# Kernel optimization log

Measured on AMD Instinct MI355X. Metric: run time of the kernel, lower is better.

## Reference

```python
import jax, jax.numpy as jnp
import numpy as np

N_USER = 200000
N_REPO = 100000
N_EDGE = 1500000
D = 128       # input feature dim for both node types
H = 128       # hidden_channels
O = 128       # out_channels


def _sage(x_src, x_dst, src_idx, dst_idx, n_dst, Wl, bl, Wr):
    # PyG SAGEConv: mean-aggregate source features per destination,
    # then lin_l(aggr) + lin_r(x_dst). lin_l has bias, lin_r does not.
    msg = x_src[src_idx]                                   # [E, d_src] gather
    s = jax.ops.segment_sum(msg, dst_idx, num_segments=n_dst)
    cnt = jax.ops.segment_sum(jnp.ones((src_idx.shape[0],), x_src.dtype),
                              dst_idx, num_segments=n_dst)
    mean = s / jnp.maximum(cnt, 1.0)[:, None]
    return mean @ Wl + bl + x_dst @ Wr


def setup_inputs() -> dict:
    key = jax.random.key(0)
    ks = jax.random.split(key, 16)
    s = 1.0 / np.sqrt(D)
    inp = {
        "x_user": jax.random.normal(ks[0], (N_USER, D), jnp.float32),
        "x_repo": jax.random.normal(ks[1], (N_REPO, D), jnp.float32),
        # row 0: user indices, row 1: repo indices
        "edge_stars": jnp.stack([
            jax.random.randint(ks[2], (N_EDGE,), 0, N_USER),
            jax.random.randint(ks[3], (N_EDGE,), 0, N_REPO),
        ]).astype(jnp.int64),
        # layer 1, edge type (user, stars, repo)
        "Wl1s": jax.random.uniform(ks[4], (D, H), jnp.float32, -s, s),
        "bl1s": jnp.zeros((H,), jnp.float32),
        "Wr1s": jax.random.uniform(ks[5], (D, H), jnp.float32, -s, s),
        # layer 1, edge type (repo, rev_stars, user)
        "Wl1r": jax.random.uniform(ks[6], (D, H), jnp.float32, -s, s),
        "bl1r": jnp.zeros((H,), jnp.float32),
        "Wr1r": jax.random.uniform(ks[7], (D, H), jnp.float32, -s, s),
        # layer 2, edge type (user, stars, repo)
        "Wl2s": jax.random.uniform(ks[8], (H, O), jnp.float32, -s, s),
        "bl2s": jnp.zeros((O,), jnp.float32),
        "Wr2s": jax.random.uniform(ks[9], (H, O), jnp.float32, -s, s),
        # layer 2, edge type (repo, rev_stars, user)
        "Wl2r": jax.random.uniform(ks[10], (H, O), jnp.float32, -s, s),
        "bl2r": jnp.zeros((O,), jnp.float32),
        "Wr2r": jax.random.uniform(ks[11], (H, O), jnp.float32, -s, s),
    }
    return inp


def reference(x_user, x_repo, edge_stars,
              Wl1s, bl1s, Wr1s, Wl1r, bl1r, Wr1r,
              Wl2s, bl2s, Wr2s, Wl2r, bl2r, Wr2r):
    u_idx, r_idx = edge_stars[0], edge_stars[1]
    # layer 1: stars (user->repo) updates repo; rev_stars (repo->user) updates user
    repo_h = jax.nn.relu(_sage(x_user, x_repo, u_idx, r_idx, N_REPO, Wl1s, bl1s, Wr1s))
    user_h = jax.nn.relu(_sage(x_repo, x_user, r_idx, u_idx, N_USER, Wl1r, bl1r, Wr1r))
    # layer 2
    repo_out = _sage(user_h, repo_h, u_idx, r_idx, N_REPO, Wl2s, bl2s, Wr2s)
    user_out = _sage(repo_h, user_h, r_idx, u_idx, N_USER, Wl2r, bl2r, Wr2r)
    return user_out, repo_out
```

## Files before the change

kernel.cpp:

```cpp
#include <hip/hip_runtime.h>
#include <stdint.h>

#define NUSER 200000
#define NREPO 100000
#define NEDGE 1500000

#define RB 98
#define UB 196
#define RCAP 17500
#define UCAP 9000

typedef unsigned short u16;
typedef unsigned int u32;
typedef __bf16 bf16x8 __attribute__((ext_vector_type(8)));
typedef float f32x4 __attribute__((ext_vector_type(4)));

#define OFF_RECR 0UL
#define OFF_RECU 6860000UL
#define OFF_B0   0UL
#define OFF_B1   51200256UL
#define OFF_B2   76800512UL
#define OFF_B3   128000768UL
#define OFF_COLR 153601024UL
#define OFF_COLU 159601024UL
#define OFF_POSR 165601024UL
#define OFF_POSU 166001024UL
#define OFF_WT   166801024UL
#define OFF_CUR  167063168UL
#define WS_NEEDED 167065568UL

#define ZR_B0 (OFF_B0 + 51200000UL)
#define ZR_B1 (OFF_B1 + 25600000UL)
#define ZR_B2 (OFF_B2 + 51200000UL)
#define ZR_B3 (OFF_B3 + 25600000UL)

__device__ __forceinline__ float bflo(u32 p) { return __uint_as_float(p << 16); }
__device__ __forceinline__ float bfhi(u32 p) { return __uint_as_float(p & 0xffff0000u); }
__device__ __forceinline__ u16 f2bf(float f) {
    u32 u = __float_as_uint(f);
    return (u16)((u + 0x7fffu + ((u >> 16) & 1u)) >> 16);
}
__device__ __forceinline__ bf16x8 as_bf16x8(uint4 u) {
    union { uint4 a; bf16x8 b; } x; x.a = u; return x.b;
}

__global__ void sentinel_kernel(float* out) { out[threadIdx.x] = 1234.5f; }

__global__ void init_kernel(char* __restrict__ ws) {
    int t = threadIdx.x;
    int* g = (int*)(ws + OFF_CUR);
    if (t < 300) g[t] = 0;
    if (t < 64) {
        ((u32*)(ws + ZR_B0))[t] = 0;
        ((u32*)(ws + ZR_B1))[t] = 0;
        ((u32*)(ws + ZR_B2))[t] = 0;
        ((u32*)(ws + ZR_B3))[t] = 0;
    }
}

__global__ void cvt_bf16_both(const float4* __restrict__ inA, uint2* __restrict__ outA, int n4A,
                              const float4* __restrict__ inB, uint2* __restrict__ outB, int n4B) {
    int i = blockIdx.x * blockDim.x + threadIdx.x;
    const float4* in; uint2* out; int idx;
    if (i < n4A) { in = inA; out = outA; idx = i; }
    else { in = inB; out = outB; idx = i - n4A; if (idx >= n4B) return; }
    float4 v = in[idx];
    uint2 o;
    o.x = (u32)f2bf(v.x) | ((u32)f2bf(v.y) << 16);
    o.y = (u32)f2bf(v.z) | ((u32)f2bf(v.w) << 16);
    out[idx] = o;
}

__global__ void wprep4_kernel(const float* __restrict__ Wl0, const float* __restrict__ Wr0,
                              const float* __restrict__ Wl1, const float* __restrict__ Wr1,
                              const float* __restrict__ Wl2, const float* __restrict__ Wr2,
                              const float* __restrict__ Wl3, const float* __restrict__ Wr3,
                              u16* __restrict__ Wt) {
    int which = blockIdx.x >> 7;
    const float* Wl = (which == 0) ? Wl0 : (which == 1) ? Wl1 : (which == 2) ? Wl2 : Wl3;
    const float* Wr = (which == 0) ? Wr0 : (which == 1) ? Wr1 : (which == 2) ? Wr2 : Wr3;
    int idx = (blockIdx.x & 127) * 256 + threadIdx.x;
    int n = idx >> 8, k = idx & 255;
    float v = (k < 128) ? Wl[k * 128 + n] : Wr[(k - 128) * 128 + n];
    Wt[which * 32768 + idx] = f2bf(v);
}

__device__ __forceinline__ bool detect_is64(const u32* e) {
    __shared__ int any_odd;
    int t = threadIdx.x;
    if (t == 0) any_odd = 0;
    __syncthreads();
    u32 acc = 0;
#pragma unroll
    for (int r = 0; r < 4; ++r) acc |= e[2 * (256 * r + t) + 1];
    if (acc != 0) any_odd = 1;
    __syncthreads();
    return !any_odd;
}

__global__ __launch_bounds__(256)
void passA_bin(const u32* __restrict__ e, u32* __restrict__ rec_r, u32* __restrict__ rec_u,
               int* __restrict__ gcur_r, int* __restrict__ gcur_u) {
    __shared__ int cntR[RB], cntU[UB], baseR[RB], baseU[UB];
    bool is64 = detect_is64(e);
    int t = threadIdx.x;
    for (int i = t; i < RB; i += 256) cntR[i] = 0;
    for (int i = t; i < UB; i += 256) cntU[i] = 0;
    __syncthreads();
    int base = blockIdx.x * 4096;
    int us[16], rs[16];
#pragma unroll
    for (int j = 0; j < 16; ++j) {
        int i = base + j * 256 + t;
        int u = -1, r = -1;
        if (i < NEDGE) {
            u = is64 ? (int)e[2 * i] : (int)e[i];
            r = is64 ? (int)e[2 * (NEDGE + i)] : (int)e[NEDGE + i];
        }
        us[j] = u; rs[j] = r;
        if (u >= 0) { atomicAdd(&cntR[r >> 10], 1); atomicAdd(&cntU[u >> 10], 1); }
    }
    __syncthreads();
    for (int i = t; i < RB; i += 256) baseR[i] = cntR[i] ? atomicAdd(&gcur_r[i], cntR[i]) : 0;
    for (int i = t; i < UB; i += 256) baseU[i] = cntU[i] ? atomicAdd(&gcur_u[i], cntU[i]) : 0;
    __syncthreads();
    for (int i = t; i < RB; i += 256) cntR[i] = 0;
    for (int i = t; i < UB; i += 256) cntU[i] = 0;
    __syncthreads();
#pragma unroll
    for (int j = 0; j < 16; ++j) {
        int u = us[j], r = rs[j];
        if (u >= 0) {
            int br = r >> 10, bu = u >> 10;
            int rk = baseR[br] + atomicAdd(&cntR[br], 1);
            if (rk < RCAP) rec_r[br * RCAP + rk] = ((u32)u << 10) | (u32)(r & 1023);
            int ku = baseU[bu] + atomicAdd(&cntU[bu], 1);
            if (ku < UCAP) rec_u[bu * UCAP + ku] = ((u32)r << 10) | (u32)(u & 1023);
        }
    }
}

__global__ void bucket_scan(const int* __restrict__ gcur_r, const int* __restrict__ gcur_u,
                            int* __restrict__ cb_r, int* __restrict__ cb_u) {
    __shared__ int s0[256], s1[256];
    int t = threadIdx.x;
    s0[t] = (t < RB) ? min(gcur_r[t], RCAP) : 0;
    __syncthreads();
    int* src = s0; int* dst = s1;
    for (int off = 1; off < 256; off <<= 1) {
        int x = src[t]; if (t >= off) x += src[t - off];
        dst[t] = x; __syncthreads();
        int* tmp = src; src = dst; dst = tmp;
    }
    if (t < RB) cb_r[t] = (t == 0) ? 0 : src[t - 1];
    __syncthreads();
    src[t] = 0; __syncthreads();
    s0[t] = (t < UB) ? min(gcur_u[t], UCAP) : 0;
    __syncthreads();
    src = s0; dst = s1;
    for (int off = 1; off < 256; off <<= 1) {
        int x = src[t]; if (t >= off) x += src[t - off];
        dst[t] = x; __syncthreads();
        int* tmp = src; src = dst; dst = tmp;
    }
    if (t < UB) cb_u[t] = (t == 0) ? 0 : src[t - 1];
}

__global__ __launch_bounds__(256)
void passB_build(const u32* __restrict__ rec_r, const u32* __restrict__ rec_u,
                 const int* __restrict__ gcur_r, const int* __restrict__ gcur_u,
                 const int* __restrict__ cb_r, const int* __restrict__ cb_u,
                 int* __restrict__ col_r, int* __restrict__ col_u,
                 int* __restrict__ pos_r, int* __restrict__ pos_u) {
    __shared__ int cnt[1024];
    __shared__ int excl[1024];
    __shared__ int sc0[256], sc1[256];
    int b = blockIdx.x;
    const u32* rec; int count, colbase, dstbase, ndst; int* col; int* pos;
    if (b < RB) {
        rec = rec_r + (size_t)b * RCAP; count = min(gcur_r[b], RCAP); colbase = cb_r[b];
        dstbase = b << 10; ndst = min(1024, NREPO - dstbase); col = col_r; pos = pos_r;
    } else {
        int c = b - RB;
        rec = rec_u + (size_t)c * UCAP; count = min(gcur_u[c], UCAP); colbase = cb_u[c];
        dstbase = c << 10; ndst = min(1024, NUSER - dstbase); col = col_u; pos = pos_u;
    }
    int t = threadIdx.x;
    for (int i = t; i < 1024; i += 256) cnt[i] = 0;
    __syncthreads();
    for (int i = t; i < count; i += 256) atomicAdd(&cnt[rec[i] & 1023], 1);
    __syncthreads();
    int c0 = cnt[t * 4], c1 = cnt[t * 4 + 1], c2 = cnt[t * 4 + 2], c3 = cnt[t * 4 + 3];
    int tsum = c0 + c1 + c2 + c3;
    sc0[t] = tsum; __syncthreads();
    int* src = sc0; int* dst = sc1;
    for (int off = 1; off < 256; off <<= 1) {
        int x = src[t]; if (t >= off) x += src[t - off];
        dst[t] = x; __syncthreads();
        int* tmp = src; src = dst; dst = tmp;
    }
    int exclT = src[t] - tsum;
    int e0 = exclT, e1 = e0 + c0, e2 = e1 + c1, e3 = e2 + c2;
    excl[t * 4] = e0; excl[t * 4 + 1] = e1; excl[t * 4 + 2] = e2; excl[t * 4 + 3] = e3;
    {
        int i = t * 4;
        if (i < ndst)     pos[dstbase + i]     = colbase + e1;
        if (i + 1 < ndst) pos[dstbase + i + 1] = colbase + e2;
        if (i + 2 < ndst) pos[dstbase + i + 2] = colbase + e3;
        if (i + 3 < ndst) pos[dstbase + i + 3] = colbase + e3 + c3;
    }
    __syncthreads();
    for (int i = t; i < 1024; i += 256) cnt[i] = 0;
    __syncthreads();
    for (int i = t; i < count; i += 256) {
        u32 rc = rec[i];
        int dl = rc & 1023;
        int rk = atomicAdd(&cnt[dl], 1);
        col[colbase + excl[dl] + rk] = (int)(rc >> 10);
    }
}

__global__ __launch_bounds__(256)
void gather_mean2(const u16* __restrict__ featA, const int* __restrict__ colA,
                  const int* __restrict__ posA, u16* __restrict__ outA, int ndstA, int nwaveA, int zrowA,
                  const u16* __restrict__ featB, const int* __restrict__ colB,
                  const int* __restrict__ posB, u16* __restrict__ outB, int ndstB, int zrowB) {
    int gw = (blockIdx.x * blockDim.x + threadIdx.x) >> 6;
    const u16* feat; const int* col; const int* pos; u16* outm; int ndst, dbase, zrow;
    if (gw < nwaveA) {
        feat = featA; col = colA; pos = posA; outm = outA; ndst = ndstA; dbase = gw * 2; zrow = zrowA;
    } else {
        feat = featB; col = colB; pos = posB; outm = outB; ndst = ndstB; dbase = (gw - nwaveA) * 2; zrow = zrowB;
    }
    int lane = threadIdx.x & 63;
    int h = lane >> 5, l5 = lane & 31, g2 = l5 >> 4, s = l5 & 15;
    int d = dbase + h;
    if (d >= ndst) return;

    int start = (d == 0) ? 0 : pos[d - 1];
    int end = pos[d];
    int deg = end - start;

    float acc[8];
#pragma unroll
    for (int k = 0; k < 8; ++k) acc[k] = 0.f;

#define LDROW(idx) (*(const uint4*)(feat + (size_t)(idx) * 128 + s * 8))
#define ACC4(a, b, c, dd) \
    acc[0] += (bflo(a.x) + bflo(b.x)) + (bflo(c.x) + bflo(dd.x)); \
    acc[1] += (bfhi(a.x) + bfhi(b.x)) + (bfhi(c.x) + bfhi(dd.x)); \
    acc[2] += (bflo(a.y) + bflo(b.y)) + (bflo(c.y) + bflo(dd.y)); \
    acc[3] += (bfhi(a.y) + bfhi(b.y)) + (bfhi(c.y) + bfhi(dd.y)); \
    acc[4] += (bflo(a.z) + bflo(b.z)) + (bflo(c.z) + bflo(dd.z)); \
    acc[5] += (bfhi(a.z) + bfhi(b.z)) + (bfhi(c.z) + bfhi(dd.z)); \
    acc[6] += (bflo(a.w) + bflo(b.w)) + (bflo(c.w) + bflo(dd.w)); \
    acc[7] += (bfhi(a.w) + bfhi(b.w)) + (bfhi(c.w) + bfhi(dd.w));

    if (deg > 0) {
        int mdeg = min(deg, 32);
        int cv = col[start + min(l5, mdeg - 1)];
        int hb = h * 32;
        for (int e0 = 0; e0 < mdeg; e0 += 8) {
            int i0 = e0 + g2, i1 = e0 + 2 + g2, i2 = e0 + 4 + g2, i3 = e0 + 6 + g2;
            int t0 = __shfl(cv, hb + i0, 64), t1 = __shfl(cv, hb + i1, 64);
            int t2 = __shfl(cv, hb + i2, 64), t3 = __shfl(cv, hb + i3, 64);
            int x0 = (i0 < deg) ? t0 : zrow, x1 = (i1 < deg) ? t1 : zrow;
            int x2 = (i2 < deg) ? t2 : zrow, x3 = (i3 < deg) ? t3 : zrow;
            uint4 v0 = LDROW(x0), v1 = LDROW(x1), v2 = LDROW(x2), v3 = LDROW(x3);
            ACC4(v0, v1, v2, v3)
        }
        for (int e = 32 + g2; e < deg; e += 2) {
            int idx = col[start + e];
            uint4 v = LDROW(idx);
            acc[0] += bflo(v.x); acc[1] += bfhi(v.x);
            acc[2] += bflo(v.y); acc[3] += bfhi(v.y);
            acc[4] += bflo(v.z); acc[5] += bfhi(v.z);
            acc[6] += bflo(v.w); acc[7] += bfhi(v.w);
        }
#pragma unroll
        for (int k = 0; k < 8; ++k) acc[k] += __shfl_xor(acc[k], 16, 64);
    }
#undef LDROW
#undef ACC4

    if (g2 == 0) {
        float inv = (deg > 0) ? 1.0f / (float)deg : 0.f;
        uint4 o;
        o.x = (u32)f2bf(acc[0] * inv) | ((u32)f2bf(acc[1] * inv) << 16);
        o.y = (u32)f2bf(acc[2] * inv) | ((u32)f2bf(acc[3] * inv) << 16);
        o.z = (u32)f2bf(acc[4] * inv) | ((u32)f2bf(acc[5] * inv) << 16);
        o.w = (u32)f2bf(acc[6] * inv) | ((u32)f2bf(acc[7] * inv) << 16);
        *(uint4*)(outm + (size_t)d * 128 + s * 8) = o;
    }
}

__global__ __launch_bounds__(256)
void transform_both(const u16* __restrict__ A_A, const u16* __restrict__ X_A,
                    const u16* __restrict__ Wt_A, const float* __restrict__ b_A,
                    u16* __restrict__ obf_A, float* __restrict__ of32_A, int N_A, int nblkA,
                    const u16* __restrict__ A_B, const u16* __restrict__ X_B,
                    const u16* __restrict__ Wt_B, const float* __restrict__ b_B,
                    u16* __restrict__ obf_B, float* __restrict__ of32_B, int N_B,
                    int do_relu) {
    __shared__ __align__(16) u16 sA[64][264];
    const u16* A; const u16* X; const u16* Wt; const float* bias;
    u16* out_bf; float* out_f32; int N, base;
    if ((int)blockIdx.x < nblkA) {
        A = A_A; X = X_A; Wt = Wt_A; bias = b_A; out_bf = obf_A; out_f32 = of32_A;
        N = N_A; base = blockIdx.x * 64;
    } else {
        A = A_B; X = X_B; Wt = Wt_B; bias = b_B; out_bf = obf_B; out_f32 = of32_B;
        N = N_B; base = (blockIdx.x - nblkA) * 64;
    }
    int tid = threadIdx.x;
    int w = tid >> 6, lane = tid & 63;
    int q = lane >> 4, n = lane & 15;
    int nb = w * 32;

    bf16x8 bfrag[2][8];
#pragma unroll
    for (int nt = 0; nt < 2; ++nt)
#pragma unroll
        for (int ks = 0; ks < 8; ++ks)
            bfrag[nt][ks] = as_bf16x8(*(const uint4*)(Wt + (size_t)(nb + nt * 16 + n) * 256 + ks * 32 + q * 8));
    float bv[2] = { bias[nb + n], bias[nb + 16 + n] };

    {
        int r = tid >> 2, c = tid & 3;
        int node = base + r;
        uint4 z = make_uint4(0, 0, 0, 0);
        uint4 va[4], vx[4];
        if (node < N) {
            const uint4* pa = (const uint4*)(A + (size_t)node * 128 + c * 32);
            const uint4* px = (const uint4*)(X + (size_t)node * 128 + c * 32);
#pragma unroll
            for (int j = 0; j < 4; ++j) { va[j] = pa[j]; vx[j] = px[j]; }
        } else {
#pragma unroll
            for (int j = 0; j < 4; ++j) { va[j] = z; vx[j] = z; }
        }
#pragma unroll
        for (int j = 0; j < 4; ++j) {
            *(uint4*)&sA[r][c * 32 + j * 8] = va[j];
            *(uint4*)&sA[r][128 + c * 32 + j * 8] = vx[j];
        }
    }
    __syncthreads();

    f32x4 zz = { 0.f, 0.f, 0.f, 0.f };
    f32x4 acc[4][2];
#pragma unroll
    for (int mt = 0; mt < 4; ++mt) { acc[mt][0] = zz; acc[mt][1] = zz; }

#pragma unroll
    for (int ks = 0; ks < 8; ++ks)
#pragma unroll
        for (int mt = 0; mt < 4; ++mt) {
            bf16x8 af = *(const bf16x8*)&sA[mt * 16 + n][ks * 32 + q * 8];
            acc[mt][0] = __builtin_amdgcn_mfma_f32_16x16x32_bf16(af, bfrag[0][ks], acc[mt][0], 0, 0, 0);
            acc[mt][1] = __builtin_amdgcn_mfma_f32_16x16x32_bf16(af, bfrag[1][ks], acc[mt][1], 0, 0, 0);
        }

#pragma unroll
    for (int mt = 0; mt < 4; ++mt) {
        int row0 = base + mt * 16 + q * 4;
#pragma unroll
        for (int nt = 0; nt < 2; ++nt) {
            int colg = nb + nt * 16 + n;
#pragma unroll
            for (int r = 0; r < 4; ++r) {
                int row = row0 + r;
                if (row < N) {
                    float v = acc[mt][nt][r] + bv[nt];
                    if (do_relu) v = fmaxf(v, 0.f);
                    if (out_bf) out_bf[(size_t)row * 128 + colg] = f2bf(v);
                    else        out_f32[(size_t)row * 128 + colg] = v;
                }
            }
        }
    }
}

extern "C" void kernel_launch(void* const* d_in, const int* in_sizes, int n_in,
                              void* d_out, int out_size, void* d_ws, size_t ws_size,
                              hipStream_t stream) {
    const float* x_user = (const float*)d_in[0];
    const float* x_repo = (const float*)d_in[1];
    const u32* edges = (const u32*)d_in[2];
    const float* Wl1s = (const float*)d_in[3], *bl1s = (const float*)d_in[4], *Wr1s = (const float*)d_in[5];
    const float* Wl1r = (const float*)d_in[6], *bl1r = (const float*)d_in[7], *Wr1r = (const float*)d_in[8];
    const float* Wl2s = (const float*)d_in[9], *bl2s = (const float*)d_in[10], *Wr2s = (const float*)d_in[11];
    const float* Wl2r = (const float*)d_in[12], *bl2r = (const float*)d_in[13], *Wr2r = (const float*)d_in[14];

    float* out_user = (float*)d_out;
    float* out_repo = (float*)d_out + (size_t)NUSER * 128;

    if (ws_size < WS_NEEDED) {
        hipLaunchKernelGGL(sentinel_kernel, dim3(1), dim3(256), 0, stream, out_user);
        return;
    }

    char* ws = (char*)d_ws;
    u32* rec_r = (u32*)(ws + OFF_RECR);
    u32* rec_u = (u32*)(ws + OFF_RECU);
    u16* B0 = (u16*)(ws + OFF_B0);
    u16* B1 = (u16*)(ws + OFF_B1);
    u16* B2 = (u16*)(ws + OFF_B2);
    u16* B3 = (u16*)(ws + OFF_B3);
    int* col_r = (int*)(ws + OFF_COLR);
    int* col_u = (int*)(ws + OFF_COLU);
    int* pos_r = (int*)(ws + OFF_POSR);
    int* pos_u = (int*)(ws + OFF_POSU);
    u16* wt1s = (u16*)(ws + OFF_WT);
    u16* wt1r = wt1s + 32768;
    u16* wt2s = wt1r + 32768;
    u16* wt2r = wt2s + 32768;
    int* gcur_r = (int*)(ws + OFF_CUR);
    int* gcur_u = (int*)(ws + OFF_CUR + 400);
    int* cb_r   = (int*)(ws + OFF_CUR + 1200);
    int* cb_u   = (int*)(ws + OFF_CUR + 1600);

    const int nblkR = (NREPO + 63) / 64;
    const int nblkU = (NUSER + 63) / 64;
    const int nwaveR = NREPO / 2;
    const int nwaveU = NUSER / 2;
    const int gblk = (nwaveR + nwaveU) / 4;

    hipLaunchKernelGGL(init_kernel, dim3(1), dim3(320), 0, stream, ws);
    hipLaunchKernelGGL(passA_bin, dim3(367), dim3(256), 0, stream, edges, rec_r, rec_u, gcur_r, gcur_u);
    hipLaunchKernelGGL(bucket_scan, dim3(1), dim3(256), 0, stream, gcur_r, gcur_u, cb_r, cb_u);
    hipLaunchKernelGGL(passB_build, dim3(RB + UB), dim3(256), 0, stream,
                       rec_r, rec_u, gcur_r, gcur_u, cb_r, cb_u, col_r, col_u, pos_r, pos_u);

    hipLaunchKernelGGL(wprep4_kernel, dim3(512), dim3(256), 0, stream,
                       Wl1s, Wr1s, Wl1r, Wr1r, Wl2s, Wr2s, Wl2r, Wr2r, wt1s);
    hipLaunchKernelGGL(cvt_bf16_both, dim3(37500), dim3(256), 0, stream,
                       (const float4*)x_user, (uint2*)B2, NUSER * 128 / 4,
                       (const float4*)x_repo, (uint2*)B3, NREPO * 128 / 4);

    hipLaunchKernelGGL(gather_mean2, dim3(gblk), dim3(256), 0, stream,
                       B2, col_r, pos_r, B1, NREPO, nwaveR, NUSER,
                       B3, col_u, pos_u, B0, NUSER, NREPO);
    hipLaunchKernelGGL(transform_both, dim3(nblkR + nblkU), dim3(256), 0, stream,
                       B1, B3, wt1s, bl1s, B1, (float*)nullptr, NREPO, nblkR,
                       B0, B2, wt1r, bl1r, B0, (float*)nullptr, NUSER,
                       1);

    hipLaunchKernelGGL(gather_mean2, dim3(gblk), dim3(256), 0, stream,
                       B0, col_r, pos_r, B3, NREPO, nwaveR, NUSER,
                       B1, col_u, pos_u, B2, NUSER, NREPO);
    hipLaunchKernelGGL(transform_both, dim3(nblkR + nblkU), dim3(256), 0, stream,
                       B3, B1, wt2s, bl2s, (u16*)nullptr, out_repo, NREPO, nblkR,
                       B2, B0, wt2r, bl2r, (u16*)nullptr, out_user, NUSER,
                       0);
}
```

Baseline: 680.2 us.

## Process multiple node tiles per transform block, shrink binning blocks, load gather indices directly

The transform kernel now handles four 64-row tiles per block and reloads the weight fragments only when the tile switches between the repo and user sides, which cuts the number of redundant weight-fragment loads. Edge binning uses 1024 edges per block instead of 4096, which launches more blocks to raise parallelism but adds more global atomics on the bucket cursors. The gather kernel reads neighbor indices straight from memory instead of broadcasting them with wave shuffles. This lowers shuffle work but issues more scattered index loads.

```diff
diff --git a/kernel.cpp b/kernel.cpp
--- a/kernel.cpp
+++ b/kernel.cpp
@@ -107,10 +107,10 @@
     for (int i = t; i < RB; i += 256) cntR[i] = 0;
     for (int i = t; i < UB; i += 256) cntU[i] = 0;
     __syncthreads();
-    int base = blockIdx.x * 4096;
-    int us[16], rs[16];
-#pragma unroll
-    for (int j = 0; j < 16; ++j) {
+    int base = blockIdx.x * 1024;
+    int us[4], rs[4];
+#pragma unroll
+    for (int j = 0; j < 4; ++j) {
         int i = base + j * 256 + t;
         int u = -1, r = -1;
         if (i < NEDGE) {
@@ -128,7 +128,7 @@
     for (int i = t; i < UB; i += 256) cntU[i] = 0;
     __syncthreads();
 #pragma unroll
-    for (int j = 0; j < 16; ++j) {
+    for (int j = 0; j < 4; ++j) {
         int u = us[j], r = rs[j];
         if (u >= 0) {
             int br = r >> 10, bu = u >> 10;
@@ -258,19 +258,17 @@
 
     if (deg > 0) {
         int mdeg = min(deg, 32);
-        int cv = col[start + min(l5, mdeg - 1)];
-        int hb = h * 32;
+        const int* cbase = col + start;
         for (int e0 = 0; e0 < mdeg; e0 += 8) {
             int i0 = e0 + g2, i1 = e0 + 2 + g2, i2 = e0 + 4 + g2, i3 = e0 + 6 + g2;
-            int t0 = __shfl(cv, hb + i0, 64), t1 = __shfl(cv, hb + i1, 64);
-            int t2 = __shfl(cv, hb + i2, 64), t3 = __shfl(cv, hb + i3, 64);
+            int t0 = cbase[i0], t1 = cbase[i1], t2 = cbase[i2], t3 = cbase[i3];
             int x0 = (i0 < deg) ? t0 : zrow, x1 = (i1 < deg) ? t1 : zrow;
             int x2 = (i2 < deg) ? t2 : zrow, x3 = (i3 < deg) ? t3 : zrow;
             uint4 v0 = LDROW(x0), v1 = LDROW(x1), v2 = LDROW(x2), v3 = LDROW(x3);
             ACC4(v0, v1, v2, v3)
         }
         for (int e = 32 + g2; e < deg; e += 2) {
-            int idx = col[start + e];
+            int idx = cbase[e];
             uint4 v = LDROW(idx);
             acc[0] += bflo(v.x); acc[1] += bfhi(v.x);
             acc[2] += bflo(v.y); acc[3] += bfhi(v.y);
@@ -294,87 +292,103 @@
     }
 }
 
+#define TILES_PER_BLK 4
 __global__ __launch_bounds__(256)
 void transform_both(const u16* __restrict__ A_A, const u16* __restrict__ X_A,
                     const u16* __restrict__ Wt_A, const float* __restrict__ b_A,
                     u16* __restrict__ obf_A, float* __restrict__ of32_A, int N_A, int nblkA,
                     const u16* __restrict__ A_B, const u16* __restrict__ X_B,
                     const u16* __restrict__ Wt_B, const float* __restrict__ b_B,
-                    u16* __restrict__ obf_B, float* __restrict__ of32_B, int N_B,
+                    u16* __restrict__ obf_B, float* __restrict__ of32_B, int N_B, int nblkB,
                     int do_relu) {
     __shared__ __align__(16) u16 sA[64][264];
-    const u16* A; const u16* X; const u16* Wt; const float* bias;
-    u16* out_bf; float* out_f32; int N, base;
-    if ((int)blockIdx.x < nblkA) {
-        A = A_A; X = X_A; Wt = Wt_A; bias = b_A; out_bf = obf_A; out_f32 = of32_A;
-        N = N_A; base = blockIdx.x * 64;
-    } else {
-        A = A_B; X = X_B; Wt = Wt_B; bias = b_B; out_bf = obf_B; out_f32 = of32_B;
-        N = N_B; base = (blockIdx.x - nblkA) * 64;
-    }
     int tid = threadIdx.x;
     int w = tid >> 6, lane = tid & 63;
     int q = lane >> 4, n = lane & 15;
     int nb = w * 32;
+    int r_st = tid >> 2, c_st = tid & 3;
 
     bf16x8 bfrag[2][8];
-#pragma unroll
-    for (int nt = 0; nt < 2; ++nt)
+    float bv[2];
+    int prev_side = -1;
+
+    int tile0 = blockIdx.x * TILES_PER_BLK;
+    int ntile = nblkA + nblkB;
+    for (int ti = 0; ti < TILES_PER_BLK; ++ti) {
+        int tile = tile0 + ti;
+        if (tile >= ntile) break;
+        int side = (tile < nblkA) ? 0 : 1;
+        const u16* A; const u16* X; const u16* Wt; const float* bias;
+        u16* out_bf; float* out_f32; int N, base;
+        if (side == 0) {
+            A = A_A; X = X_A; Wt = Wt_A; bias = b_A; out_bf = obf_A; out_f32 = of32_A;
+            N = N_A; base = tile * 64;
+        } else {
+            A = A_B; X = X_B; Wt = Wt_B; bias = b_B; out_bf = obf_B; out_f32 = of32_B;
+            N = N_B; base = (tile - nblkA) * 64;
+        }
+
+        if (side != prev_side) {
+            prev_side = side;
+#pragma unroll
+            for (int nt = 0; nt < 2; ++nt)
+#pragma unroll
+                for (int ks = 0; ks < 8; ++ks)
+                    bfrag[nt][ks] = as_bf16x8(*(const uint4*)(Wt + (size_t)(nb + nt * 16 + n) * 256 + ks * 32 + q * 8));
+            bv[0] = bias[nb + n]; bv[1] = bias[nb + 16 + n];
+        }
+
+        if (ti > 0) __syncthreads();
+        {
+            int node = base + r_st;
+            uint4 z = make_uint4(0, 0, 0, 0);
+            uint4 va[4], vx[4];
+            if (node < N) {
+                const uint4* pa = (const uint4*)(A + (size_t)node * 128 + c_st * 32);
+                const uint4* px = (const uint4*)(X + (size_t)node * 128 + c_st * 32);
+#pragma unroll
+                for (int j = 0; j < 4; ++j) { va[j] = pa[j]; vx[j] = px[j]; }
+            } else {
+#pragma unroll
+                for (int j = 0; j < 4; ++j) { va[j] = z; vx[j] = z; }
+            }
+#pragma unroll
+            for (int j = 0; j < 4; ++j) {
+                *(uint4*)&sA[r_st][c_st * 32 + j * 8] = va[j];
+                *(uint4*)&sA[r_st][128 + c_st * 32 + j * 8] = vx[j];
+            }
+        }
+        __syncthreads();
+
+        f32x4 zz = { 0.f, 0.f, 0.f, 0.f };
+        f32x4 acc[4][2];
+#pragma unroll
+        for (int mt = 0; mt < 4; ++mt) { acc[mt][0] = zz; acc[mt][1] = zz; }
+
 #pragma unroll
         for (int ks = 0; ks < 8; ++ks)
-            bfrag[nt][ks] = as_bf16x8(*(const uint4*)(Wt + (size_t)(nb + nt * 16 + n) * 256 + ks * 32 + q * 8));
-    float bv[2] = { bias[nb + n], bias[nb + 16 + n] };
-
-    {
-        int r = tid >> 2, c = tid & 3;
-        int node = base + r;
-        uint4 z = make_uint4(0, 0, 0, 0);
-        uint4 va[4], vx[4];
-        if (node < N) {
-            const uint4* pa = (const uint4*)(A + (size_t)node * 128 + c * 32);
-            const uint4* px = (const uint4*)(X + (size_t)node * 128 + c * 32);
-#pragma unroll
-            for (int j = 0; j < 4; ++j) { va[j] = pa[j]; vx[j] = px[j]; }
-        } else {
-#pragma unroll
-            for (int j = 0; j < 4; ++j) { va[j] = z; vx[j] = z; }
-        }
-#pragma unroll
-        for (int j = 0; j < 4; ++j) {
-            *(uint4*)&sA[r][c * 32 + j * 8] = va[j];
-            *(uint4*)&sA[r][128 + c * 32 + j * 8] = vx[j];
-        }
-    }
-    __syncthreads();
-
-    f32x4 zz = { 0.f, 0.f, 0.f, 0.f };
-    f32x4 acc[4][2];
-#pragma unroll
-    for (int mt = 0; mt < 4; ++mt) { acc[mt][0] = zz; acc[mt][1] = zz; }
-
-#pragma unroll
-    for (int ks = 0; ks < 8; ++ks)
+#pragma unroll
+            for (int mt = 0; mt < 4; ++mt) {
+                bf16x8 af = *(const bf16x8*)&sA[mt * 16 + n][ks * 32 + q * 8];
+                acc[mt][0] = __builtin_amdgcn_mfma_f32_16x16x32_bf16(af, bfrag[0][ks], acc[mt][0], 0, 0, 0);
+                acc[mt][1] = __builtin_amdgcn_mfma_f32_16x16x32_bf16(af, bfrag[1][ks], acc[mt][1], 0, 0, 0);
+            }
+
 #pragma unroll
         for (int mt = 0; mt < 4; ++mt) {
-            bf16x8 af = *(const bf16x8*)&sA[mt * 16 + n][ks * 32 + q * 8];
-            acc[mt][0] = __builtin_amdgcn_mfma_f32_16x16x32_bf16(af, bfrag[0][ks], acc[mt][0], 0, 0, 0);
-            acc[mt][1] = __builtin_amdgcn_mfma_f32_16x16x32_bf16(af, bfrag[1][ks], acc[mt][1], 0, 0, 0);
-        }
-
-#pragma unroll
-    for (int mt = 0; mt < 4; ++mt) {
-        int row0 = base + mt * 16 + q * 4;
-#pragma unroll
-        for (int nt = 0; nt < 2; ++nt) {
-            int colg = nb + nt * 16 + n;
-#pragma unroll
-            for (int r = 0; r < 4; ++r) {
-                int row = row0 + r;
-                if (row < N) {
-                    float v = acc[mt][nt][r] + bv[nt];
-                    if (do_relu) v = fmaxf(v, 0.f);
-                    if (out_bf) out_bf[(size_t)row * 128 + colg] = f2bf(v);
-                    else        out_f32[(size_t)row * 128 + colg] = v;
+            int row0 = base + mt * 16 + q * 4;
+#pragma unroll
+            for (int nt = 0; nt < 2; ++nt) {
+                int colg = nb + nt * 16 + n;
+#pragma unroll
+                for (int r = 0; r < 4; ++r) {
+                    int row = row0 + r;
+                    if (row < N) {
+                        float v = acc[mt][nt][r] + bv[nt];
+                        if (do_relu) v = fmaxf(v, 0.f);
+                        if (out_bf) out_bf[(size_t)row * 128 + colg] = f2bf(v);
+                        else        out_f32[(size_t)row * 128 + colg] = v;
+                    }
                 }
             }
         }
@@ -422,12 +436,15 @@
 
     const int nblkR = (NREPO + 63) / 64;
     const int nblkU = (NUSER + 63) / 64;
+    const int ntile = nblkR + nblkU;
+    const int tblk = (ntile + TILES_PER_BLK - 1) / TILES_PER_BLK;
     const int nwaveR = NREPO / 2;
     const int nwaveU = NUSER / 2;
     const int gblk = (nwaveR + nwaveU) / 4;
 
     hipLaunchKernelGGL(init_kernel, dim3(1), dim3(320), 0, stream, ws);
-    hipLaunchKernelGGL(passA_bin, dim3(367), dim3(256), 0, stream, edges, rec_r, rec_u, gcur_r, gcur_u);
+    hipLaunchKernelGGL(passA_bin, dim3((NEDGE + 1023) / 1024), dim3(256), 0, stream,
+                       edges, rec_r, rec_u, gcur_r, gcur_u);
     hipLaunchKernelGGL(bucket_scan, dim3(1), dim3(256), 0, stream, gcur_r, gcur_u, cb_r, cb_u);
     hipLaunchKernelGGL(passB_build, dim3(RB + UB), dim3(256), 0, stream,
                        rec_r, rec_u, gcur_r, gcur_u, cb_r, cb_u, col_r, col_u, pos_r, pos_u);
@@ -441,16 +458,16 @@
     hipLaunchKernelGGL(gather_mean2, dim3(gblk), dim3(256), 0, stream,
                        B2, col_r, pos_r, B1, NREPO, nwaveR, NUSER,
                        B3, col_u, pos_u, B0, NUSER, NREPO);
-    hipLaunchKernelGGL(transform_both, dim3(nblkR + nblkU), dim3(256), 0, stream,
+    hipLaunchKernelGGL(transform_both, dim3(tblk), dim3(256), 0, stream,
                        B1, B3, wt1s, bl1s, B1, (float*)nullptr, NREPO, nblkR,
-                       B0, B2, wt1r, bl1r, B0, (float*)nullptr, NUSER,
+                       B0, B2, wt1r, bl1r, B0, (float*)nullptr, NUSER, nblkU,
                        1);
 
     hipLaunchKernelGGL(gather_mean2, dim3(gblk), dim3(256), 0, stream,
                        B0, col_r, pos_r, B3, NREPO, nwaveR, NUSER,
                        B1, col_u, pos_u, B2, NUSER, NREPO);
-    hipLaunchKernelGGL(transform_both, dim3(nblkR + nblkU), dim3(256), 0, stream,
+    hipLaunchKernelGGL(transform_both, dim3(tblk), dim3(256), 0, stream,
                        B3, B1, wt2s, bl2s, (u16*)nullptr, out_repo, NREPO, nblkR,
-                       B2, B0, wt2r, bl2r, (u16*)nullptr, out_user, NUSER,
+                       B2, B0, wt2r, bl2r, (u16*)nullptr, out_user, NUSER, nblkU,
                        0);
 }
```

Result: slower. 701.9 us (+3.2%).
